# Performance work log

Hardware: AMD Instinct MI355X
Metric: run time of the kernel (lower is better)

## Reference

```python
import jax, jax.numpy as jnp
import numpy as np

# Static per-expert capacities (tokens are laid out contiguously per expert)
CAPS = [1024, 512, 1024, 256, 1024, 512, 128, 1024, 512, 1024, 256, 512, 1024, 128, 64, 512]
TOTAL = sum(CAPS)  # 9536
E, H, I = 16, 1024, 4096
OFFSETS = np.concatenate([[0], np.cumsum(CAPS)])


def setup_inputs() -> dict:
    key = jax.random.key(0)
    ks = jax.random.split(key, 5)
    x = jax.random.normal(ks[0], (TOTAL, H), dtype=jnp.float32)
    W1 = jax.random.normal(ks[1], (E, I, H), dtype=jnp.float32) * 0.02
    b1 = jax.random.normal(ks[2], (E, I), dtype=jnp.float32) * 0.02
    W2 = jax.random.normal(ks[3], (E, H, I), dtype=jnp.float32) * 0.02
    b2 = jax.random.normal(ks[4], (E, H), dtype=jnp.float32) * 0.02
    return {"x": x, "W1": W1, "b1": b1, "W2": W2, "b2": b2}


def reference(x, W1, b1, W2, b2):
    # Grouped GEMM FFN: expert e processes rows [OFFSETS[e]:OFFSETS[e+1]]
    # out = gelu(x_e @ W1[e].T + b1[e]) @ W2[e].T + b2[e]
    outs = []
    for e in range(E):  # fixed, static loop over experts (capacities are static)
        xs = x[OFFSETS[e]:OFFSETS[e + 1]]                      # [cap_e, H]
        h = jax.nn.gelu(xs @ W1[e].T + b1[e], approximate=False)  # [cap_e, I]
        outs.append(h @ W2[e].T + b2[e])                       # [cap_e, H]
    return jnp.concatenate(outs, axis=0)                       # [TOTAL, H]
```

## Files before the change

kernel.cpp:

```cpp
#include <hip/hip_runtime.h>
#include <math.h>

typedef __attribute__((ext_vector_type(8))) short short8;
typedef __attribute__((ext_vector_type(4))) float f32x4;
typedef __attribute__((ext_vector_type(4))) float float4v;
typedef __attribute__((ext_vector_type(4))) unsigned short ushort4v;

#define E_NUM 16

__constant__ int d_caps[E_NUM] = {1024,512,1024,256,1024,512,128,1024,512,1024,256,512,1024,128,64,512};
__constant__ int d_offs[E_NUM] = {0,1024,1536,2560,2816,3840,4352,4480,5504,6016,7040,7296,7808,8832,8960,9024};

__device__ __forceinline__ unsigned short bf16_of(float f){
  unsigned int u = __builtin_bit_cast(unsigned int, f);
  return (unsigned short)((u + 0x7FFFu + ((u >> 16) & 1u)) >> 16);
}

template<bool A_BF16, bool GELU_OUT, int NDIM, int KDIM, int LOG_NTN>
__global__ __launch_bounds__(256, 2)
void expert_gemm(const void* __restrict__ Av, const float* __restrict__ W,
                 const float* __restrict__ bias, void* __restrict__ Outv)
{
  __shared__ __align__(16) unsigned short smem[16384];
  unsigned short* a_lds = smem;
  unsigned short* b_lds = smem + 8192;

  const int tid = threadIdx.x;
  const int bid = blockIdx.x;

  int e = 0, m0 = 0, n0 = 0;
  {
    int acc = 0;
    #pragma unroll
    for (int i = 0; i < E_NUM; ++i) {
      int mt = (d_caps[i] + 127) >> 7;
      int nb = mt << LOG_NTN;
      if (bid >= acc && bid < acc + nb) {
        e = i;
        int loc = bid - acc;
        m0 = (loc >> LOG_NTN) * 128;
        n0 = (loc & ((1 << LOG_NTN) - 1)) * 128;
      }
      acc += nb;
    }
  }
  const int Me   = d_caps[e];
  const int tok0 = d_offs[e];
  const float* Wb = W + (size_t)e * NDIM * KDIM;

  const int sr  = tid >> 3;
  const int skq = (tid & 7) * 4;
  const int hr  = tid >> 2;
  const int hc  = (tid & 3) * 8;

  const float*          Af = (const float*)Av;
  const unsigned short* Ah = (const unsigned short*)Av;

  float4v ra[4]; short8 ha[2]; float4v rb[4];

  auto load_tile = [&](int kt) {
    const int k0 = kt * 32;
    if (A_BF16) {
      #pragma unroll
      for (int i = 0; i < 2; ++i) {
        int grow = m0 + hr + 64 * i;
        if (grow < Me)
          ha[i] = *reinterpret_cast<const short8*>(Ah + (size_t)(tok0 + grow) * KDIM + k0 + hc);
        else
          ha[i] = (short8){0,0,0,0,0,0,0,0};
      }
    } else {
      #pragma unroll
      for (int i = 0; i < 4; ++i) {
        int grow = m0 + sr + 32 * i;
        if (grow < Me)
          ra[i] = *reinterpret_cast<const float4v*>(Af + (size_t)(tok0 + grow) * KDIM + k0 + skq);
        else
          ra[i] = (float4v){0.f,0.f,0.f,0.f};
      }
    }
    #pragma unroll
    for (int i = 0; i < 4; ++i) {
      int row = sr + 32 * i;
      rb[i] = *reinterpret_cast<const float4v*>(Wb + (size_t)(n0 + row) * KDIM + k0 + skq);
    }
  };

  auto write_tile = [&](int buf) {
    unsigned short* ab = a_lds + buf * 4096;
    unsigned short* bb = b_lds + buf * 4096;
    if (A_BF16) {
      #pragma unroll
      for (int i = 0; i < 2; ++i) {
        int row = hr + 64 * i;
        *reinterpret_cast<short8*>(ab + row * 32 + hc) = ha[i];
      }
    } else {
      #pragma unroll
      for (int i = 0; i < 4; ++i) {
        int row = sr + 32 * i;
        ushort4v p;
        p[0] = bf16_of(ra[i][0]); p[1] = bf16_of(ra[i][1]);
        p[2] = bf16_of(ra[i][2]); p[3] = bf16_of(ra[i][3]);
        *reinterpret_cast<ushort4v*>(ab + row * 32 + skq) = p;
      }
    }
    #pragma unroll
    for (int i = 0; i < 4; ++i) {
      int row = sr + 32 * i;
      ushort4v p;
      p[0] = bf16_of(rb[i][0]); p[1] = bf16_of(rb[i][1]);
      p[2] = bf16_of(rb[i][2]); p[3] = bf16_of(rb[i][3]);
      *reinterpret_cast<ushort4v*>(bb + row * 32 + skq) = p;
    }
  };

  const int lane = tid & 63;
  const int wv   = tid >> 6;
  const int wm   = (wv >> 1) * 64;
  const int wn   = (wv & 1) * 64;
  const int lrow = lane & 15;
  const int kcol = (lane >> 4) * 8;

  f32x4 acc_[4][4];
  #pragma unroll
  for (int i = 0; i < 4; ++i)
    #pragma unroll
    for (int j = 0; j < 4; ++j)
      acc_[i][j] = (f32x4){0.f,0.f,0.f,0.f};

  load_tile(0);
  write_tile(0);
  __syncthreads();

  const int NT = KDIM / 32;
  for (int kt = 0; kt < NT; ++kt) {
    const int cur = kt & 1;
    if (kt + 1 < NT) load_tile(kt + 1);

    const unsigned short* ab = a_lds + cur * 4096;
    const unsigned short* bb = b_lds + cur * 4096;
    short8 afr[4], bfr[4];
    #pragma unroll
    for (int f = 0; f < 4; ++f)
      afr[f] = *reinterpret_cast<const short8*>(ab + (wm + f * 16 + lrow) * 32 + kcol);
    #pragma unroll
    for (int f = 0; f < 4; ++f)
      bfr[f] = *reinterpret_cast<const short8*>(bb + (wn + f * 16 + lrow) * 32 + kcol);

    #pragma unroll
    for (int i = 0; i < 4; ++i)
      #pragma unroll
      for (int j = 0; j < 4; ++j)
        acc_[i][j] = __builtin_amdgcn_mfma_f32_16x16x32_bf16(afr[i], bfr[j], acc_[i][j], 0, 0, 0);

    if (kt + 1 < NT) write_tile(cur ^ 1);
    __syncthreads();
  }

  float bv[4];
  #pragma unroll
  for (int f = 0; f < 4; ++f)
    bv[f] = bias[(size_t)e * NDIM + n0 + wn + f * 16 + lrow];

  if (GELU_OUT) {
    unsigned short* hout = smem;
    #pragma unroll
    for (int i = 0; i < 4; ++i) {
      const int rbase = wm + i * 16 + (lane >> 4) * 4;
      #pragma unroll
      for (int j = 0; j < 4; ++j) {
        #pragma unroll
        for (int jj = 0; jj < 4; ++jj) {
          float xv = acc_[i][j][jj] + bv[j];
          float g  = 0.5f * xv * (1.0f + erff(xv * 0.70710678118654752f));
          hout[(rbase + jj) * 128 + wn + j * 16 + lrow] = bf16_of(g);
        }
      }
    }
    __syncthreads();
    unsigned short* Oh = (unsigned short*)Outv;
    #pragma unroll
    for (int it = 0; it < 8; ++it) {
      int row  = it * 16 + (tid >> 4);
      int c    = (tid & 15) * 8;
      int grow = m0 + row;
      if (grow < Me) {
        *reinterpret_cast<short8*>(Oh + (size_t)(tok0 + grow) * NDIM + n0 + c)
          = *reinterpret_cast<const short8*>(hout + row * 128 + c);
      }
    }
  } else {
    float* Of = (float*)Outv;
    #pragma unroll
    for (int i = 0; i < 4; ++i) {
      const int rbase = wm + i * 16 + (lane >> 4) * 4;
      #pragma unroll
      for (int jj = 0; jj < 4; ++jj) {
        int grow = m0 + rbase + jj;
        if (grow < Me) {
          #pragma unroll
          for (int j = 0; j < 4; ++j) {
            Of[(size_t)(tok0 + grow) * NDIM + n0 + wn + j * 16 + lrow] = acc_[i][j][jj] + bv[j];
          }
        }
      }
    }
  }
}

extern "C" void kernel_launch(void* const* d_in, const int* in_sizes, int n_in,
                              void* d_out, int out_size, void* d_ws, size_t ws_size,
                              hipStream_t stream)
{
  const float* x  = (const float*)d_in[0];
  const float* W1 = (const float*)d_in[1];
  const float* b1 = (const float*)d_in[2];
  const float* W2 = (const float*)d_in[3];
  const float* b2 = (const float*)d_in[4];
  float* out = (float*)d_out;
  unsigned short* h = (unsigned short*)d_ws;

  constexpr int MT_TILES = 75;

  expert_gemm<false, true, 4096, 1024, 5><<<MT_TILES * 32, 256, 0, stream>>>(
      (const void*)x, W1, b1, (void*)h);

  expert_gemm<true, false, 1024, 4096, 3><<<MT_TILES * 8, 256, 0, stream>>>(
      (const void*)h, W2, b2, (void*)out);
}
```

Baseline: 446.7 us.

## Swizzle tiles across XCDs, pad LDS, use 64-row tiles for second GEMM

Remaps block IDs so consecutive tiles are spread across the 8 XCDs and grouped along N for L2 reuse of weights. LDS rows are padded to a stride of 40 to reduce bank conflicts, and bf16 conversion now uses the hardware v_cvt_pk_bf16_f32 instruction. The second GEMM switches to 64-row M tiles to launch more blocks, and launch bounds rise to 4 blocks per CU. Row bounds checks on loads are removed, which relies on every expert capacity being a multiple of the tile height; the GELU store now uses round-to-nearest conversion from the hardware instruction.

```diff
diff --git a/kernel.cpp b/kernel.cpp
--- a/kernel.cpp
+++ b/kernel.cpp
@@ -3,50 +3,62 @@
 
 typedef __attribute__((ext_vector_type(8))) short short8;
 typedef __attribute__((ext_vector_type(4))) float f32x4;
-typedef __attribute__((ext_vector_type(4))) float float4v;
-typedef __attribute__((ext_vector_type(4))) unsigned short ushort4v;
+typedef __attribute__((ext_vector_type(2))) unsigned int u32x2;
 
 #define E_NUM 16
-
-__constant__ int d_caps[E_NUM] = {1024,512,1024,256,1024,512,128,1024,512,1024,256,512,1024,128,64,512};
-__constant__ int d_offs[E_NUM] = {0,1024,1536,2560,2816,3840,4352,4480,5504,6016,7040,7296,7808,8832,8960,9024};
-
-__device__ __forceinline__ unsigned short bf16_of(float f){
-  unsigned int u = __builtin_bit_cast(unsigned int, f);
-  return (unsigned short)((u + 0x7FFFu + ((u >> 16) & 1u)) >> 16);
+constexpr int CAPS[E_NUM] = {1024,512,1024,256,1024,512,128,1024,512,1024,256,512,1024,128,64,512};
+constexpr int OFFS[E_NUM] = {0,1024,1536,2560,2816,3840,4352,4480,5504,6016,7040,7296,7808,8832,8960,9024};
+constexpr int cdiv_(int a, int b){ return (a + b - 1) / b; }
+constexpr int ilog2_(int v){ int l = 0; while ((1 << l) < v) ++l; return l; }
+
+__device__ __forceinline__ unsigned int cvt_pk_bf16(float a, float b){
+  unsigned int r;
+  asm("v_cvt_pk_bf16_f32 %0, %1, %2" : "=v"(r) : "v"(a), "v"(b));
+  return r;
 }
 
-template<bool A_BF16, bool GELU_OUT, int NDIM, int KDIM, int LOG_NTN>
-__global__ __launch_bounds__(256, 2)
+template<bool A_BF16, bool GELU_OUT, int TM, int NDIM, int KDIM, int LOG_GN, int NWG>
+__global__ __launch_bounds__(256, 4)
 void expert_gemm(const void* __restrict__ Av, const float* __restrict__ W,
                  const float* __restrict__ bias, void* __restrict__ Outv)
 {
-  __shared__ __align__(16) unsigned short smem[16384];
-  unsigned short* a_lds = smem;
-  unsigned short* b_lds = smem + 8192;
-
-  const int tid = threadIdx.x;
-  const int bid = blockIdx.x;
-
-  int e = 0, m0 = 0, n0 = 0;
+  constexpr int STR  = 40;
+  constexpr int A_SZ = TM * STR;
+  constexpr int B_SZ = 128 * STR;
+  constexpr int GN   = 1 << LOG_GN;
+  constexpr int MFR  = TM / 32;
+  static_assert(NWG % 8 == 0, "grid must be divisible by 8 for XCD swizzle");
+
+  __shared__ __align__(16) unsigned short smem[2 * A_SZ + 2 * B_SZ];
+
+  const int tid  = threadIdx.x;
+  const int braw = blockIdx.x;
+  const int t = (braw & 7) * (NWG / 8) + (braw >> 3);
+
+  int m0 = 0, n0 = 0, Me = 0, tok0 = 0;
+  size_t wbase = 0, bbase = 0;
   {
-    int acc = 0;
+    int acc0 = 0;
     #pragma unroll
     for (int i = 0; i < E_NUM; ++i) {
-      int mt = (d_caps[i] + 127) >> 7;
-      int nb = mt << LOG_NTN;
-      if (bid >= acc && bid < acc + nb) {
-        e = i;
-        int loc = bid - acc;
-        m0 = (loc >> LOG_NTN) * 128;
-        n0 = (loc & ((1 << LOG_NTN) - 1)) * 128;
-      }
-      acc += nb;
+      const int mt  = cdiv_(CAPS[i], TM);
+      const int lmt = ilog2_(mt);
+      const int nb  = mt * (NDIM / 128);
+      if (t >= acc0 && t < acc0 + nb) {
+        const int loc = t - acc0;
+        const int g   = loc >> (lmt + LOG_GN);
+        const int rem = loc & ((mt << LOG_GN) - 1);
+        m0   = (rem >> LOG_GN) * TM;
+        n0   = ((g << LOG_GN) | (rem & (GN - 1))) * 128;
+        Me   = CAPS[i];
+        tok0 = OFFS[i];
+        wbase = (size_t)i * NDIM * KDIM;
+        bbase = (size_t)i * NDIM;
+      }
+      acc0 += nb;
     }
   }
-  const int Me   = d_caps[e];
-  const int tok0 = d_offs[e];
-  const float* Wb = W + (size_t)e * NDIM * KDIM;
+  const float* Wb = W + wbase;
 
   const int sr  = tid >> 3;
   const int skq = (tid & 7) * 4;
@@ -56,100 +68,87 @@
   const float*          Af = (const float*)Av;
   const unsigned short* Ah = (const unsigned short*)Av;
 
-  float4v ra[4]; short8 ha[2]; float4v rb[4];
+  f32x4 ra[4]; short8 ha[2]; f32x4 rb[4];
 
   auto load_tile = [&](int kt) {
     const int k0 = kt * 32;
-    if (A_BF16) {
-      #pragma unroll
-      for (int i = 0; i < 2; ++i) {
-        int grow = m0 + hr + 64 * i;
-        if (grow < Me)
-          ha[i] = *reinterpret_cast<const short8*>(Ah + (size_t)(tok0 + grow) * KDIM + k0 + hc);
-        else
-          ha[i] = (short8){0,0,0,0,0,0,0,0};
-      }
+    if constexpr (A_BF16) {
+      #pragma unroll
+      for (int i = 0; i < TM / 64; ++i)
+        ha[i] = *reinterpret_cast<const short8*>(
+            Ah + (size_t)(tok0 + m0 + hr + 64 * i) * KDIM + k0 + hc);
     } else {
       #pragma unroll
-      for (int i = 0; i < 4; ++i) {
-        int grow = m0 + sr + 32 * i;
-        if (grow < Me)
-          ra[i] = *reinterpret_cast<const float4v*>(Af + (size_t)(tok0 + grow) * KDIM + k0 + skq);
-        else
-          ra[i] = (float4v){0.f,0.f,0.f,0.f};
+      for (int i = 0; i < TM / 32; ++i)
+        ra[i] = *reinterpret_cast<const f32x4*>(
+            Af + (size_t)(tok0 + m0 + sr + 32 * i) * KDIM + k0 + skq);
+    }
+    #pragma unroll
+    for (int i = 0; i < 4; ++i)
+      rb[i] = *reinterpret_cast<const f32x4*>(
+          Wb + (size_t)(n0 + sr + 32 * i) * KDIM + k0 + skq);
+  };
+
+  auto write_tile = [&](int buf) {
+    unsigned short* ab = smem + buf * A_SZ;
+    unsigned short* bb = smem + 2 * A_SZ + buf * B_SZ;
+    if constexpr (A_BF16) {
+      #pragma unroll
+      for (int i = 0; i < TM / 64; ++i)
+        *reinterpret_cast<short8*>(ab + (hr + 64 * i) * STR + hc) = ha[i];
+    } else {
+      #pragma unroll
+      for (int i = 0; i < TM / 32; ++i) {
+        u32x2 p;
+        p[0] = cvt_pk_bf16(ra[i][0], ra[i][1]);
+        p[1] = cvt_pk_bf16(ra[i][2], ra[i][3]);
+        *reinterpret_cast<u32x2*>(ab + (sr + 32 * i) * STR + skq) = p;
       }
     }
     #pragma unroll
     for (int i = 0; i < 4; ++i) {
-      int row = sr + 32 * i;
-      rb[i] = *reinterpret_cast<const float4v*>(Wb + (size_t)(n0 + row) * KDIM + k0 + skq);
-    }
-  };
-
-  auto write_tile = [&](int buf) {
-    unsigned short* ab = a_lds + buf * 4096;
-    unsigned short* bb = b_lds + buf * 4096;
-    if (A_BF16) {
-      #pragma unroll
-      for (int i = 0; i < 2; ++i) {
-        int row = hr + 64 * i;
-        *reinterpret_cast<short8*>(ab + row * 32 + hc) = ha[i];
-      }
-    } else {
-      #pragma unroll
-      for (int i = 0; i < 4; ++i) {
-        int row = sr + 32 * i;
-        ushort4v p;
-        p[0] = bf16_of(ra[i][0]); p[1] = bf16_of(ra[i][1]);
-        p[2] = bf16_of(ra[i][2]); p[3] = bf16_of(ra[i][3]);
-        *reinterpret_cast<ushort4v*>(ab + row * 32 + skq) = p;
-      }
-    }
-    #pragma unroll
-    for (int i = 0; i < 4; ++i) {
-      int row = sr + 32 * i;
-      ushort4v p;
-      p[0] = bf16_of(rb[i][0]); p[1] = bf16_of(rb[i][1]);
-      p[2] = bf16_of(rb[i][2]); p[3] = bf16_of(rb[i][3]);
-      *reinterpret_cast<ushort4v*>(bb + row * 32 + skq) = p;
+      u32x2 p;
+      p[0] = cvt_pk_bf16(rb[i][0], rb[i][1]);
+      p[1] = cvt_pk_bf16(rb[i][2], rb[i][3]);
+      *reinterpret_cast<u32x2*>(bb + (sr + 32 * i) * STR + skq) = p;
     }
   };
 
   const int lane = tid & 63;
   const int wv   = tid >> 6;
-  const int wm   = (wv >> 1) * 64;
+  const int wm   = (wv >> 1) * (TM / 2);
   const int wn   = (wv & 1) * 64;
   const int lrow = lane & 15;
   const int kcol = (lane >> 4) * 8;
 
-  f32x4 acc_[4][4];
+  f32x4 acc_[MFR][4];
   #pragma unroll
-  for (int i = 0; i < 4; ++i)
+  for (int i = 0; i < MFR; ++i)
     #pragma unroll
     for (int j = 0; j < 4; ++j)
-      acc_[i][j] = (f32x4){0.f,0.f,0.f,0.f};
+      acc_[i][j] = (f32x4){0.f, 0.f, 0.f, 0.f};
 
   load_tile(0);
   write_tile(0);
   __syncthreads();
 
-  const int NT = KDIM / 32;
+  constexpr int NT = KDIM / 32;
   for (int kt = 0; kt < NT; ++kt) {
     const int cur = kt & 1;
     if (kt + 1 < NT) load_tile(kt + 1);
 
-    const unsigned short* ab = a_lds + cur * 4096;
-    const unsigned short* bb = b_lds + cur * 4096;
-    short8 afr[4], bfr[4];
+    const unsigned short* ab = smem + cur * A_SZ;
+    const unsigned short* bb = smem + 2 * A_SZ + cur * B_SZ;
+    short8 afr[MFR], bfr[4];
+    #pragma unroll
+    for (int f = 0; f < MFR; ++f)
+      afr[f] = *reinterpret_cast<const short8*>(ab + (wm + f * 16 + lrow) * STR + kcol);
     #pragma unroll
     for (int f = 0; f < 4; ++f)
-      afr[f] = *reinterpret_cast<const short8*>(ab + (wm + f * 16 + lrow) * 32 + kcol);
-    #pragma unroll
-    for (int f = 0; f < 4; ++f)
-      bfr[f] = *reinterpret_cast<const short8*>(bb + (wn + f * 16 + lrow) * 32 + kcol);
-
-    #pragma unroll
-    for (int i = 0; i < 4; ++i)
+      bfr[f] = *reinterpret_cast<const short8*>(bb + (wn + f * 16 + lrow) * STR + kcol);
+
+    #pragma unroll
+    for (int i = 0; i < MFR; ++i)
       #pragma unroll
       for (int j = 0; j < 4; ++j)
         acc_[i][j] = __builtin_amdgcn_mfma_f32_16x16x32_bf16(afr[i], bfr[j], acc_[i][j], 0, 0, 0);
@@ -161,12 +160,13 @@
   float bv[4];
   #pragma unroll
   for (int f = 0; f < 4; ++f)
-    bv[f] = bias[(size_t)e * NDIM + n0 + wn + f * 16 + lrow];
-
-  if (GELU_OUT) {
+    bv[f] = bias[bbase + n0 + wn + f * 16 + lrow];
+
+  if constexpr (GELU_OUT) {
+    static_assert(TM == 128, "GELU path assumes 128-row tiles");
     unsigned short* hout = smem;
     #pragma unroll
-    for (int i = 0; i < 4; ++i) {
+    for (int i = 0; i < MFR; ++i) {
       const int rbase = wm + i * 16 + (lane >> 4) * 4;
       #pragma unroll
       for (int j = 0; j < 4; ++j) {
@@ -174,7 +174,7 @@
         for (int jj = 0; jj < 4; ++jj) {
           float xv = acc_[i][j][jj] + bv[j];
           float g  = 0.5f * xv * (1.0f + erff(xv * 0.70710678118654752f));
-          hout[(rbase + jj) * 128 + wn + j * 16 + lrow] = bf16_of(g);
+          hout[(rbase + jj) * 128 + wn + j * 16 + lrow] = (unsigned short)(cvt_pk_bf16(g, g) & 0xFFFFu);
         }
       }
     }
@@ -193,7 +193,7 @@
   } else {
     float* Of = (float*)Outv;
     #pragma unroll
-    for (int i = 0; i < 4; ++i) {
+    for (int i = 0; i < MFR; ++i) {
       const int rbase = wm + i * 16 + (lane >> 4) * 4;
       #pragma unroll
       for (int jj = 0; jj < 4; ++jj) {
@@ -221,11 +221,9 @@
   float* out = (float*)d_out;
   unsigned short* h = (unsigned short*)d_ws;
 
-  constexpr int MT_TILES = 75;
-
-  expert_gemm<false, true, 4096, 1024, 5><<<MT_TILES * 32, 256, 0, stream>>>(
-      (const void*)x, W1, b1, (void*)h);
-
-  expert_gemm<true, false, 1024, 4096, 3><<<MT_TILES * 8, 256, 0, stream>>>(
-      (const void*)h, W2, b2, (void*)out);
+  expert_gemm<false, true, 128, 4096, 1024, 2, 75 * 32>
+      <<<75 * 32, 256, 0, stream>>>((const void*)x, W1, b1, (void*)h);
+
+  expert_gemm<true, false, 64, 1024, 4096, 1, 149 * 8>
+      <<<149 * 8, 256, 0, stream>>>((const void*)h, W2, b2, (void*)out);
 }
```

Result: no change. 443.5 us (-0.7%).
